# Optimization experiments

Hardware: AMD Instinct MI355X
Metric: run time of the kernel (lower is better)

## Reference

```python
import jax, jax.numpy as jnp
import numpy as np


def setup_inputs() -> dict:
    key = jax.random.key(0)
    ks = jax.random.split(key, 5)
    B, D, W = 8, 768, 128
    scale = 1.0 / np.sqrt(D)
    return {
        "x": jax.random.normal(ks[0], (B, D, W, W), dtype=jnp.float32),
        "in_proj_w": jax.random.normal(ks[1], (3 * D, D), dtype=jnp.float32) * scale,
        "in_proj_b": jax.random.normal(ks[2], (3 * D,), dtype=jnp.float32) * 0.01,
        "out_w": jax.random.normal(ks[3], (D, D), dtype=jnp.float32) * scale,
        "out_b": jax.random.normal(ks[4], (D,), dtype=jnp.float32) * 0.01,
        "num_heads": 12,
        "num_tokens": 8,
    }


def reference(x, in_proj_w, in_proj_b, out_w, out_b, num_heads, num_tokens):
    B, D, Wd, Hd = x.shape
    nt = num_tokens
    gs = Hd // nt            # grid (block) size
    T = nt * nt              # number of blocks / queries
    S = gs * gs              # k/v tokens per block
    h = num_heads
    hd = D // h

    # ---- query: adaptive avg pool to (nt, nt), flatten, permute -> (B, T, D)
    q = x.reshape(B, D, nt, gs, nt, gs).mean(axis=(3, 5))      # (B, D, nt, nt)
    q = q.reshape(B, D, T).transpose(0, 2, 1)                   # (B, T, D)

    # ---- key/value: faithful reproduction of unfold + view(x.size()) + reshape
    # torch: kv_perm (B,W,H,D) -> unfold -> (B, nt, nt, D, gs, gs) contiguous,
    # then reinterpreted flat as (B, W*H, D) (scrambles channel/pixel layout).
    t = x.transpose(0, 2, 3, 1)                                 # (B, W, H, D)
    t = t.reshape(B, nt, gs, nt, gs, D).transpose(0, 1, 3, 5, 2, 4)  # (B,nt,nt,D,gs,gs)
    kv = t.reshape(B, T, S, D)                                  # chunked into T blocks of S tokens

    # ---- in-projections (torch MultiheadAttention packed weights)
    Wq, Wk, Wv = in_proj_w[:D], in_proj_w[D:2 * D], in_proj_w[2 * D:]
    bq, bk, bv = in_proj_b[:D], in_proj_b[D:2 * D], in_proj_b[2 * D:]
    qp = (q @ Wq.T + bq).reshape(B, T, h, hd)                   # (B, T, h, hd)
    kp = (kv @ Wk.T + bk).reshape(B, T, S, h, hd)               # (B, T, S, h, hd)
    vp = (kv @ Wv.T + bv).reshape(B, T, S, h, hd)

    # ---- block-local single-query attention, batched over all T blocks
    scores = jnp.einsum("bthd,btshd->bths", qp, kp) / np.sqrt(hd)  # (B, T, h, S)
    attn = jax.nn.softmax(scores, axis=-1)
    ctx = jnp.einsum("bths,btshd->bthd", attn, vp).reshape(B, T, D)

    # ---- out projection
    return ctx @ out_w.T + out_b                                # (B, T, D)
```

## Files before the change

kernel.cpp:

```cpp
#include <hip/hip_runtime.h>
#include <hip/hip_bf16.h>

#define D_ 768
#define W_ 128
#define T_ 64
#define S_ 256
#define H_ 12
#define BT_ 512

__device__ __forceinline__ unsigned short f2bf(float f) {
  unsigned u = __float_as_uint(f);
  u = (u + 0x7FFFu + ((u >> 16) & 1u)) >> 16;
  return (unsigned short)u;
}

__global__ __launch_bounds__(512) void k_pack(const float* __restrict__ x,
                                              unsigned short* __restrict__ packed,
                                              float* __restrict__ q) {
  const int blk  = blockIdx.x;
  const int cc   = blk & 15;
  const int tjp  = (blk >> 4) & 3;
  const int ti   = (blk >> 6) & 7;
  const int b    = blk >> 9;
  const int tid  = threadIdx.x;
  const int w    = tid >> 6, lane = tid & 63;
  const int btg0 = b*64 + ti*8 + tjp*2;
  const int ch0  = cc * 48;

  __shared__ unsigned short tile[48][2][260];
  __shared__ float poolacc[48][2][2];

  const float* xrow = x + (size_t)b*D_*16384 + (16*ti)*128 + 32*tjp;

  #pragma unroll
  for (int it = 0; it < 12; ++it) {
    const int idx = it*512 + tid;
    const int c8 = idx & 7;
    const int r  = (idx >> 3) & 15;
    const int ch = idx >> 7;
    const float4 v = *(const float4*)(xrow + (size_t)(ch0 + ch)*16384 + r*128 + c8*4);
    const int btl = c8 >> 2;
    const int px  = r*16 + (c8 & 3)*4;
    unsigned lo = (unsigned)f2bf(v.x) | ((unsigned)f2bf(v.y) << 16);
    unsigned hi = (unsigned)f2bf(v.z) | ((unsigned)f2bf(v.w) << 16);
    *(uint2*)&tile[ch][btl][px] = make_uint2(lo, hi);
    float ps = (v.x + v.y) + (v.z + v.w);
    ps += __shfl_xor(ps, 1);
    ps += __shfl_xor(ps, 2);
    ps += __shfl_xor(ps, 8);
    ps += __shfl_xor(ps, 16);
    ps += __shfl_xor(ps, 32);
    if (lane == 0 || lane == 4) {
      const int chw = it*4 + (w >> 1);
      const int hwv = w & 1;
      poolacc[chw][lane >> 2][hwv] = ps;
    }
  }
  __syncthreads();

  {
    const int btl = tid >> 8, p = tid & 255;
    unsigned short* pbt = packed + ((size_t)(btg0 + btl)*16 + cc)*D_*16;
    #pragma unroll
    for (int c = 0; c < 3; ++c) {
      unsigned u[8];
      #pragma unroll
      for (int k2 = 0; k2 < 8; ++k2) {
        const unsigned a  = tile[3*(2*k2)     + c][btl][p];
        const unsigned b2 = tile[3*(2*k2 + 1) + c][btl][p];
        u[k2] = a | (b2 << 16);
      }
      unsigned short* dst = pbt + (size_t)(c*256 + p)*16;
      *(uint4*)(dst)     = make_uint4(u[0], u[1], u[2], u[3]);
      *(uint4*)(dst + 8) = make_uint4(u[4], u[5], u[6], u[7]);
    }
    if (tid < 96) {
      const int ch = tid >> 1, bl = tid & 1;
      q[(size_t)(btg0 + bl)*D_ + ch0 + ch] =
          (poolacc[ch][bl][0] + poolacc[ch][bl][1]) * (1.0f/256.0f);
    }
  }
}

__global__ __launch_bounds__(256) void k_qp(const float* __restrict__ q,
                                            const float* __restrict__ ipw,
                                            const float* __restrict__ ipb,
                                            float* __restrict__ qp) {
  const int jt = blockIdx.x >> 5;
  const int bt0 = (blockIdx.x & 31) * 16;
  const int tid = threadIdx.x;
  const float* Wr = ipw + (size_t)jt*64*D_;
  __shared__ float wt[64][65];
  __shared__ float at[16][65];
  const int i = tid & 63, qw = tid >> 6;
  float acc[4] = {0,0,0,0};
  for (int dc = 0; dc < D_; dc += 64) {
    #pragma unroll
    for (int k = 0; k < 4; ++k) {
      const int idx = k*256 + tid;
      const int r = idx >> 4, c4 = idx & 15;
      *(float4*)&wt[r][c4*4] = *(const float4*)(Wr + (size_t)r*D_ + dc + c4*4);
    }
    {
      const int r = tid >> 4, c4 = tid & 15;
      *(float4*)&at[r][c4*4] = *(const float4*)(q + (size_t)(bt0 + r)*D_ + dc + c4*4);
    }
    __syncthreads();
    #pragma unroll
    for (int dd = 0; dd < 64; ++dd) {
      const float wv = wt[i][dd];
      #pragma unroll
      for (int k = 0; k < 4; ++k)
        acc[k] += at[qw + k*4][dd] * wv;
    }
    __syncthreads();
  }
  const float bqv = ipb[jt*64 + i];
  #pragma unroll
  for (int k = 0; k < 4; ++k)
    qp[(size_t)(bt0 + qw + k*4)*D_ + jt*64 + i] = acc[k] + bqv;
}

__global__ __launch_bounds__(256) void k_fold(const float* __restrict__ qp,
                                              const float* __restrict__ ipw,
                                              float* __restrict__ qkout) {
  const int btc = blockIdx.x & 15;
  const int nt  = blockIdx.x >> 4;
  const int h   = nt / 12;
  const int ddc = (nt % 12) * 64;
  const int bt0 = btc * 32;
  const int tid = threadIdx.x;
  __shared__ float qpl[32][68];
  __shared__ float wkl[64][68];
  #pragma unroll
  for (int k = 0; k < 2; ++k) {
    const int idx = k*256 + tid;
    const int r = idx >> 4, c4 = idx & 15;
    *(float4*)&qpl[r][c4*4] = *(const float4*)(qp + (size_t)(bt0 + r)*D_ + h*64 + c4*4);
  }
  #pragma unroll
  for (int k = 0; k < 4; ++k) {
    const int idx = k*256 + tid;
    const int r = idx >> 4, c4 = idx & 15;
    *(float4*)&wkl[r][c4*4] = *(const float4*)(ipw + (size_t)(D_ + h*64 + r)*D_ + ddc + c4*4);
  }
  __syncthreads();
  const int i = tid & 63, qw = tid >> 6;
  float acc[8] = {0,0,0,0,0,0,0,0};
  #pragma unroll 8
  for (int kk = 0; kk < 64; ++kk) {
    const float w = wkl[kk][i];
    #pragma unroll
    for (int k = 0; k < 8; ++k)
      acc[k] += qpl[qw + k*4][kk] * w;
  }
  #pragma unroll
  for (int k = 0; k < 8; ++k)
    qkout[((size_t)(bt0 + qw + k*4)*H_ + h)*D_ + ddc + i] = acc[k] * 0.125f;
}

__global__ __launch_bounds__(256) void k_attn3(const unsigned short* __restrict__ packed,
                                               const float* __restrict__ qkin,
                                               float* __restrict__ wout) {
  const int bt = blockIdx.x;
  const int tid = threadIdx.x;
  const int wv = tid >> 6, lane = tid & 63;
  __shared__ float qk_lds[H_*D_];
  __shared__ float sc[H_][S_];

  {
    const float4* src = (const float4*)(qkin + (size_t)bt*H_*D_);
    float4* dst = (float4*)qk_lds;
    #pragma unroll
    for (int k = 0; k < 9; ++k) dst[k*256 + tid] = src[k*256 + tid];
  }
  __syncthreads();

  float acc[H_][4];
  #pragma unroll
  for (int h = 0; h < H_; ++h)
    #pragma unroll
    for (int j = 0; j < 4; ++j) acc[h][j] = 0.f;

  {
    const unsigned short* pb = packed + ((size_t)bt*16 + (lane >> 2))*D_*16 + (lane & 3)*4;
    const int d0 = wv * 192;
    #pragma unroll 4
    for (int d4 = 0; d4 < 48; ++d4) {
      const int d = d0 + d4*4;
      float f[4][4];
      #pragma unroll
      for (int dd = 0; dd < 4; ++dd) {
        const short4 pv = *(const short4*)(pb + (size_t)(d + dd)*16);
        f[dd][0] = __uint_as_float(((unsigned)(unsigned short)pv.x) << 16);
        f[dd][1] = __uint_as_float(((unsigned)(unsigned short)pv.y) << 16);
        f[dd][2] = __uint_as_float(((unsigned)(unsigned short)pv.z) << 16);
        f[dd][3] = __uint_as_float(((unsigned)(unsigned short)pv.w) << 16);
      }
      #pragma unroll
      for (int h = 0; h < H_; ++h) {
        const float4 qv = *(const float4*)&qk_lds[h*D_ + d];
        #pragma unroll
        for (int j = 0; j < 4; ++j)
          acc[h][j] += qv.x*f[0][j] + qv.y*f[1][j] + qv.z*f[2][j] + qv.w*f[3][j];
      }
    }
  }
  __syncthreads();

  if (wv == 0) {
    #pragma unroll
    for (int h = 0; h < H_; ++h)
      *(float4*)&sc[h][lane*4] = make_float4(acc[h][0], acc[h][1], acc[h][2], acc[h][3]);
  } else {
    float* dstp = qk_lds + (size_t)(wv - 1)*(H_*S_);
    #pragma unroll
    for (int h = 0; h < H_; ++h)
      *(float4*)&dstp[h*S_ + lane*4] = make_float4(acc[h][0], acc[h][1], acc[h][2], acc[h][3]);
  }
  __syncthreads();
  #pragma unroll
  for (int h = 0; h < H_; ++h)
    sc[h][tid] += qk_lds[0*(H_*S_) + h*S_ + tid]
                + qk_lds[1*(H_*S_) + h*S_ + tid]
                + qk_lds[2*(H_*S_) + h*S_ + tid];
  __syncthreads();

  {
    #pragma unroll
    for (int hh = 0; hh < 3; ++hh) {
      const int h = wv*3 + hh;
      float4 v = *(const float4*)(&sc[h][lane*4]);
      float m = fmaxf(fmaxf(v.x, v.y), fmaxf(v.z, v.w));
      #pragma unroll
      for (int off = 32; off > 0; off >>= 1) m = fmaxf(m, __shfl_xor(m, off));
      const float e0 = __expf(v.x - m), e1 = __expf(v.y - m),
                  e2 = __expf(v.z - m), e3 = __expf(v.w - m);
      float ss = (e0+e1)+(e2+e3);
      #pragma unroll
      for (int off = 32; off > 0; off >>= 1) ss += __shfl_xor(ss, off);
      const float inv = 1.0f / ss;
      *(float4*)(&sc[h][lane*4]) = make_float4(e0*inv, e1*inv, e2*inv, e3*inv);
    }
  }
  __syncthreads();

  float wacc[H_][3];
  #pragma unroll
  for (int h = 0; h < H_; ++h) { wacc[h][0]=0.f; wacc[h][1]=0.f; wacc[h][2]=0.f; }
  const unsigned short* prow = packed + (size_t)bt*16*D_*16;
  #pragma unroll 2
  for (int s8 = 0; s8 < 32; ++s8) {
    float f[3][8];
    #pragma unroll
    for (int c = 0; c < 3; ++c) {
      const uint4 pv = *(const uint4*)(prow + ((size_t)(s8 >> 1)*D_ + c*256 + tid)*16
                                            + (s8 & 1)*8);
      f[c][0] = __uint_as_float(pv.x << 16);
      f[c][1] = __uint_as_float(pv.x & 0xFFFF0000u);
      f[c][2] = __uint_as_float(pv.y << 16);
      f[c][3] = __uint_as_float(pv.y & 0xFFFF0000u);
      f[c][4] = __uint_as_float(pv.z << 16);
      f[c][5] = __uint_as_float(pv.z & 0xFFFF0000u);
      f[c][6] = __uint_as_float(pv.w << 16);
      f[c][7] = __uint_as_float(pv.w & 0xFFFF0000u);
    }
    #pragma unroll
    for (int h = 0; h < H_; ++h) {
      const float4 a0 = *(const float4*)&sc[h][s8*8];
      const float4 a1 = *(const float4*)&sc[h][s8*8 + 4];
      #pragma unroll
      for (int c = 0; c < 3; ++c)
        wacc[h][c] += a0.x*f[c][0] + a0.y*f[c][1] + a0.z*f[c][2] + a0.w*f[c][3]
                    + a1.x*f[c][4] + a1.y*f[c][5] + a1.z*f[c][6] + a1.w*f[c][7];
    }
  }
  float* wp = wout + (size_t)bt*H_*D_;
  #pragma unroll
  for (int h = 0; h < H_; ++h)
    #pragma unroll
    for (int c = 0; c < 3; ++c)
      wp[h*D_ + c*256 + tid] = wacc[h][c];
}

__global__ __launch_bounds__(256) void k_q(const float* __restrict__ x, float* __restrict__ q) {
  const int bd = blockIdx.x;
  const int tid = threadIdx.x;
  const float4* xp = (const float4*)(x + (size_t)bd * (W_*W_));
  float acc[8] = {0,0,0,0,0,0,0,0};
  #pragma unroll
  for (int k = 0; k < 16; ++k) {
    float4 v = xp[k*256 + tid];
    acc[k>>1] += (v.x + v.y) + (v.z + v.w);
  }
  __shared__ float part[256][9];
  #pragma unroll
  for (int i = 0; i < 8; ++i) part[tid][i] = acc[i];
  __syncthreads();
  if (tid < 64) {
    const int ti = tid >> 3, tj = tid & 7;
    float s = 0.f;
    #pragma unroll
    for (int m = 0; m < 8; ++m)
      #pragma unroll
      for (int n = 0; n < 4; ++n)
        s += part[m*32 + tj*4 + n][ti];
    const int b = bd / D_, d = bd - b*D_;
    q[(size_t)(b*T_ + tid)*D_ + d] = s * (1.0f/256.0f);
  }
}

__global__ __launch_bounds__(256) void k_attn(const float* __restrict__ x,
                                              const float* __restrict__ qkin,
                                              float* __restrict__ wout) {
  const int bt = blockIdx.x;
  const int b = bt >> 6, t = bt & 63;
  const int ti = t >> 3, tj = t & 7;
  const int tid = threadIdx.x;
  __shared__ float qkl[H_*D_];
  __shared__ float sc[H_][S_];
  const float* xb = x + (size_t)b*D_*W_*W_ + ti*16*W_ + tj*16;
  {
    const float4* src = (const float4*)(qkin + (size_t)bt*H_*D_);
    float4* dst = (float4*)qkl;
    #pragma unroll
    for (int k = 0; k < 9; ++k) dst[k*256 + tid] = src[k*256 + tid];
  }
  __syncthreads();
  float acc[H_];
  #pragma unroll
  for (int h = 0; h < H_; ++h) acc[h] = 0.f;
  #pragma unroll
  for (int c = 0; c < 3; ++c) {
    const float* chp = xb + (size_t)(3*tid + c)*(W_*W_);
    for (int blk = 0; blk < 8; ++blk) {
      float4 v[8];
      #pragma unroll
      for (int u = 0; u < 8; ++u) {
        const int pg = blk*8 + u;
        v[u] = *(const float4*)(chp + (pg>>2)*W_ + (pg&3)*4);
      }
      const int dbase = c*256 + blk*32;
      #pragma unroll
      for (int h = 0; h < H_; ++h) {
        const float4* qh = (const float4*)(qkl + h*D_ + dbase);
        float s0 = 0.f;
        #pragma unroll
        for (int u = 0; u < 8; ++u) {
          const float4 qq = qh[u];
          s0 += qq.x*v[u].x + qq.y*v[u].y + qq.z*v[u].z + qq.w*v[u].w;
        }
        acc[h] += s0;
      }
    }
  }
  #pragma unroll
  for (int h = 0; h < H_; ++h) sc[h][tid] = acc[h];
  __syncthreads();
  {
    const int wv = tid >> 6, lane = tid & 63;
    #pragma unroll
    for (int hh = 0; hh < 3; ++hh) {
      const int h = wv*3 + hh;
      float4 v = *(const float4*)(&sc[h][lane*4]);
      float m = fmaxf(fmaxf(v.x, v.y), fmaxf(v.z, v.w));
      #pragma unroll
      for (int off = 32; off > 0; off >>= 1) m = fmaxf(m, __shfl_xor(m, off));
      const float e0 = __expf(v.x - m), e1 = __expf(v.y - m),
                  e2 = __expf(v.z - m), e3 = __expf(v.w - m);
      float ss = (e0+e1)+(e2+e3);
      #pragma unroll
      for (int off = 32; off > 0; off >>= 1) ss += __shfl_xor(ss, off);
      const float inv = 1.0f / ss;
      *(float4*)(&sc[h][lane*4]) = make_float4(e0*inv, e1*inv, e2*inv, e3*inv);
    }
  }
  __syncthreads();
  float wacc[H_][3];
  #pragma unroll
  for (int h = 0; h < H_; ++h) { wacc[h][0]=0.f; wacc[h][1]=0.f; wacc[h][2]=0.f; }
  const float* xp0 = xb + (tid>>4)*W_ + (tid&15);
  for (int s = 0; s < S_; ++s) {
    const float p0 = xp0[(size_t)(3*s+0)*(W_*W_)];
    const float p1 = xp0[(size_t)(3*s+1)*(W_*W_)];
    const float p2 = xp0[(size_t)(3*s+2)*(W_*W_)];
    #pragma unroll
    for (int h = 0; h < H_; ++h) {
      const float at = sc[h][s];
      wacc[h][0] += at*p0; wacc[h][1] += at*p1; wacc[h][2] += at*p2;
    }
  }
  float* wp = wout + (size_t)bt*H_*D_;
  #pragma unroll
  for (int h = 0; h < H_; ++h)
    #pragma unroll
    for (int c = 0; c < 3; ++c)
      wp[h*D_ + c*256 + tid] = wacc[h][c];
}

__global__ __launch_bounds__(256) void k_ctx(const float* __restrict__ wbuf,
                                             const float* __restrict__ ipw,
                                             const float* __restrict__ ipb,
                                             float* __restrict__ ctx) {
  const int h = blockIdx.x >> 5;
  const int bt0 = (blockIdx.x & 31) * 16;
  const int tid = threadIdx.x;
  const float* Wv = ipw + (size_t)2*D_*D_ + (size_t)h*64*D_;
  __shared__ float wt[64][65];
  __shared__ float at[16][65];
  const int i = tid & 63, qw = tid >> 6;
  float acc[4] = {0,0,0,0};
  for (int dc = 0; dc < D_; dc += 64) {
    #pragma unroll
    for (int k = 0; k < 4; ++k) {
      const int idx = k*256 + tid;
      const int r = idx >> 4, c4 = idx & 15;
      *(float4*)&wt[r][c4*4] = *(const float4*)(Wv + (size_t)r*D_ + dc + c4*4);
    }
    {
      const int r = tid >> 4, c4 = tid & 15;
      *(float4*)&at[r][c4*4] = *(const float4*)(wbuf + ((size_t)(bt0 + r)*H_ + h)*D_ + dc + c4*4);
    }
    __syncthreads();
    #pragma unroll
    for (int dd = 0; dd < 64; ++dd) {
      const float wv = wt[i][dd];
      #pragma unroll
      for (int k = 0; k < 4; ++k)
        acc[k] += at[qw + k*4][dd] * wv;
    }
    __syncthreads();
  }
  const float bvv = ipb[2*D_ + h*64 + i];
  #pragma unroll
  for (int k = 0; k < 4; ++k)
    ctx[(size_t)(bt0 + qw + k*4)*D_ + h*64 + i] = acc[k] + bvv;
}

__global__ __launch_bounds__(256) void k_out(const float* __restrict__ ctx,
                                             const float* __restrict__ ow,
                                             const float* __restrict__ ob,
                                             float* __restrict__ out) {
  const int jt = blockIdx.x >> 5;
  const int bt0 = (blockIdx.x & 31) * 16;
  const int tid = threadIdx.x;
  const float* Wr = ow + (size_t)jt*64*D_;
  __shared__ float wt[64][65];
  __shared__ float at[16][65];
  const int i = tid & 63, qw = tid >> 6;
  float acc[4] = {0,0,0,0};
  for (int dc = 0; dc < D_; dc += 64) {
    #pragma unroll
    for (int k = 0; k < 4; ++k) {
      const int idx = k*256 + tid;
      const int r = idx >> 4, c4 = idx & 15;
      *(float4*)&wt[r][c4*4] = *(const float4*)(Wr + (size_t)r*D_ + dc + c4*4);
    }
    {
      const int r = tid >> 4, c4 = tid & 15;
      *(float4*)&at[r][c4*4] = *(const float4*)(ctx + (size_t)(bt0 + r)*D_ + dc + c4*4);
    }
    __syncthreads();
    #pragma unroll
    for (int dd = 0; dd < 64; ++dd) {
      const float wv = wt[i][dd];
      #pragma unroll
      for (int k = 0; k < 4; ++k)
        acc[k] += at[qw + k*4][dd] * wv;
    }
    __syncthreads();
  }
  const float obv = ob[jt*64 + i];
  #pragma unroll
  for (int k = 0; k < 4; ++k)
    out[(size_t)(bt0 + qw + k*4)*D_ + jt*64 + i] = acc[k] + obv;
}

extern "C" void kernel_launch(void* const* d_in, const int* in_sizes, int n_in,
                              void* d_out, int out_size, void* d_ws, size_t ws_size,
                              hipStream_t stream) {
  const float* x   = (const float*)d_in[0];
  const float* ipw = (const float*)d_in[1];
  const float* ipb = (const float*)d_in[2];
  const float* ow  = (const float*)d_in[3];
  const float* ob  = (const float*)d_in[4];
  float* out = (float*)d_out;

  float* q    = (float*)d_ws;
  float* qp   = q    + (size_t)BT_*D_;
  float* qk   = qp   + (size_t)BT_*D_;
  float* wb   = qk   + (size_t)BT_*H_*D_;
  float* ctxb = wb   + (size_t)BT_*H_*D_;
  unsigned short* packed = (unsigned short*)(ctxb + (size_t)BT_*D_);

  const size_t need_main = ((size_t)BT_*D_*3 + (size_t)BT_*H_*D_*2) * 4
                         + (size_t)BT_*D_*S_*2;

  if (ws_size >= need_main) {
    k_pack <<<dim3(4096), dim3(512), 0, stream>>>(x, packed, q);
    k_qp   <<<dim3(384),  dim3(256), 0, stream>>>(q, ipw, ipb, qp);
    k_fold <<<dim3(2304), dim3(256), 0, stream>>>(qp, ipw, qk);
    k_attn3<<<dim3(BT_),  dim3(256), 0, stream>>>(packed, qk, wb);
    k_ctx  <<<dim3(384),  dim3(256), 0, stream>>>(wb, ipw, ipb, ctxb);
    k_out  <<<dim3(384),  dim3(256), 0, stream>>>(ctxb, ow, ob, out);
  } else {
    k_q    <<<dim3(8*D_), dim3(256), 0, stream>>>(x, q);
    k_qp   <<<dim3(384),  dim3(256), 0, stream>>>(q, ipw, ipb, qp);
    k_fold <<<dim3(2304), dim3(256), 0, stream>>>(qp, ipw, qk);
    k_attn <<<dim3(BT_),  dim3(256), 0, stream>>>(x, qk, wb);
    k_ctx  <<<dim3(384),  dim3(256), 0, stream>>>(wb, ipw, ipb, ctxb);
    k_out  <<<dim3(384),  dim3(256), 0, stream>>>(ctxb, ow, ob, out);
  }
}
```

Baseline: 413.0 us.

## Split attention heads across two blocks, store folded queries as bf16, simplify pack

The attention kernel now handles six heads per block and launches twice as many blocks. This raises occupancy through lower register and LDS use per block and spreads the work over more CUs, at the cost of reading the packed K/V stream twice. The folded query-key vectors are stored as bf16 to halve that traffic and are expanded to fp32 in LDS, which adds a rounding error. The pack kernel is reworked so each thread owns one channel column, uses 384 threads and pools with fewer shuffles.

```diff
diff --git a/kernel.cpp b/kernel.cpp
--- a/kernel.cpp
+++ b/kernel.cpp
@@ -6,6 +6,7 @@
 #define T_ 64
 #define S_ 256
 #define H_ 12
+#define HH_ 6
 #define BT_ 512
 
 __device__ __forceinline__ unsigned short f2bf(float f) {
@@ -13,8 +14,11 @@
   u = (u + 0x7FFFu + ((u >> 16) & 1u)) >> 16;
   return (unsigned short)u;
 }
-
-__global__ __launch_bounds__(512) void k_pack(const float* __restrict__ x,
+__device__ __forceinline__ float bfu(unsigned s) {
+  return __uint_as_float(s << 16);
+}
+
+__global__ __launch_bounds__(384) void k_pack(const float* __restrict__ x,
                                               unsigned short* __restrict__ packed,
                                               float* __restrict__ q) {
   const int blk  = blockIdx.x;
@@ -23,62 +27,53 @@
   const int ti   = (blk >> 6) & 7;
   const int b    = blk >> 9;
   const int tid  = threadIdx.x;
-  const int w    = tid >> 6, lane = tid & 63;
+  const int c8   = tid & 7;
+  const int ch   = tid >> 3;
+  const int btl  = c8 >> 2;
   const int btg0 = b*64 + ti*8 + tjp*2;
   const int ch0  = cc * 48;
 
   __shared__ unsigned short tile[48][2][260];
-  __shared__ float poolacc[48][2][2];
-
-  const float* xrow = x + (size_t)b*D_*16384 + (16*ti)*128 + 32*tjp;
-
-  #pragma unroll
-  for (int it = 0; it < 12; ++it) {
-    const int idx = it*512 + tid;
-    const int c8 = idx & 7;
-    const int r  = (idx >> 3) & 15;
-    const int ch = idx >> 7;
-    const float4 v = *(const float4*)(xrow + (size_t)(ch0 + ch)*16384 + r*128 + c8*4);
-    const int btl = c8 >> 2;
-    const int px  = r*16 + (c8 & 3)*4;
+  __shared__ float poolsc[48][2];
+
+  const float* xcol = x + (size_t)b*D_*16384 + (size_t)(ch0 + ch)*16384
+                        + (16*ti)*128 + 32*tjp + c8*4;
+
+  float psum = 0.f;
+  #pragma unroll
+  for (int r = 0; r < 16; ++r) {
+    const float4 v = *(const float4*)(xcol + r*128);
+    const int px = r*16 + (c8 & 3)*4;
     unsigned lo = (unsigned)f2bf(v.x) | ((unsigned)f2bf(v.y) << 16);
     unsigned hi = (unsigned)f2bf(v.z) | ((unsigned)f2bf(v.w) << 16);
     *(uint2*)&tile[ch][btl][px] = make_uint2(lo, hi);
-    float ps = (v.x + v.y) + (v.z + v.w);
-    ps += __shfl_xor(ps, 1);
-    ps += __shfl_xor(ps, 2);
-    ps += __shfl_xor(ps, 8);
-    ps += __shfl_xor(ps, 16);
-    ps += __shfl_xor(ps, 32);
-    if (lane == 0 || lane == 4) {
-      const int chw = it*4 + (w >> 1);
-      const int hwv = w & 1;
-      poolacc[chw][lane >> 2][hwv] = ps;
-    }
-  }
-  __syncthreads();
-
-  {
-    const int btl = tid >> 8, p = tid & 255;
-    unsigned short* pbt = packed + ((size_t)(btg0 + btl)*16 + cc)*D_*16;
+    psum += (v.x + v.y) + (v.z + v.w);
+  }
+  psum += __shfl_xor(psum, 1);
+  psum += __shfl_xor(psum, 2);
+  if ((c8 & 3) == 0) poolsc[ch][btl] = psum;
+  __syncthreads();
+
+  for (int ii = tid; ii < 512; ii += 384) {
+    const int bl = ii >> 8, p = ii & 255;
+    unsigned short* pbt = packed + ((size_t)(btg0 + bl)*16 + cc)*D_*16;
     #pragma unroll
     for (int c = 0; c < 3; ++c) {
       unsigned u[8];
       #pragma unroll
       for (int k2 = 0; k2 < 8; ++k2) {
-        const unsigned a  = tile[3*(2*k2)     + c][btl][p];
-        const unsigned b2 = tile[3*(2*k2 + 1) + c][btl][p];
+        const unsigned a  = tile[3*(2*k2)     + c][bl][p];
+        const unsigned b2 = tile[3*(2*k2 + 1) + c][bl][p];
         u[k2] = a | (b2 << 16);
       }
       unsigned short* dst = pbt + (size_t)(c*256 + p)*16;
       *(uint4*)(dst)     = make_uint4(u[0], u[1], u[2], u[3]);
       *(uint4*)(dst + 8) = make_uint4(u[4], u[5], u[6], u[7]);
     }
-    if (tid < 96) {
-      const int ch = tid >> 1, bl = tid & 1;
-      q[(size_t)(btg0 + bl)*D_ + ch0 + ch] =
-          (poolacc[ch][bl][0] + poolacc[ch][bl][1]) * (1.0f/256.0f);
-    }
+  }
+  if (tid < 96) {
+    const int ch2 = tid >> 1, bl = tid & 1;
+    q[(size_t)(btg0 + bl)*D_ + ch0 + ch2] = poolsc[ch2][bl] * (1.0f/256.0f);
   }
 }
 
@@ -123,7 +118,7 @@
 
 __global__ __launch_bounds__(256) void k_fold(const float* __restrict__ qp,
                                               const float* __restrict__ ipw,
-                                              float* __restrict__ qkout) {
+                                              unsigned short* __restrict__ qkout) {
   const int btc = blockIdx.x & 15;
   const int nt  = blockIdx.x >> 4;
   const int h   = nt / 12;
@@ -156,29 +151,39 @@
   }
   #pragma unroll
   for (int k = 0; k < 8; ++k)
-    qkout[((size_t)(bt0 + qw + k*4)*H_ + h)*D_ + ddc + i] = acc[k] * 0.125f;
+    qkout[((size_t)(bt0 + qw + k*4)*H_ + h)*D_ + ddc + i] = f2bf(acc[k] * 0.125f);
 }
 
 __global__ __launch_bounds__(256) void k_attn3(const unsigned short* __restrict__ packed,
-                                               const float* __restrict__ qkin,
+                                               const unsigned short* __restrict__ qkin,
                                                float* __restrict__ wout) {
-  const int bt = blockIdx.x;
+  const int hg = blockIdx.x >> 9;
+  const int bt = blockIdx.x & 511;
   const int tid = threadIdx.x;
   const int wv = tid >> 6, lane = tid & 63;
-  __shared__ float qk_lds[H_*D_];
-  __shared__ float sc[H_][S_];
+  __shared__ float pool_lds[HH_ * D_];
+  __shared__ float sc[HH_][S_];
 
   {
-    const float4* src = (const float4*)(qkin + (size_t)bt*H_*D_);
-    float4* dst = (float4*)qk_lds;
-    #pragma unroll
-    for (int k = 0; k < 9; ++k) dst[k*256 + tid] = src[k*256 + tid];
-  }
-  __syncthreads();
-
-  float acc[H_][4];
-  #pragma unroll
-  for (int h = 0; h < H_; ++h)
+    const uint4* src = (const uint4*)(qkin + ((size_t)bt*H_ + hg*HH_)*D_);
+    #pragma unroll
+    for (int k = 0; k < 3; ++k) {
+      const int idx = k*256 + tid;
+      if (idx < 576) {
+        const uint4 v = src[idx];
+        float* d = pool_lds + idx*8;
+        d[0] = bfu(v.x & 0xFFFFu); d[1] = bfu(v.x >> 16);
+        d[2] = bfu(v.y & 0xFFFFu); d[3] = bfu(v.y >> 16);
+        d[4] = bfu(v.z & 0xFFFFu); d[5] = bfu(v.z >> 16);
+        d[6] = bfu(v.w & 0xFFFFu); d[7] = bfu(v.w >> 16);
+      }
+    }
+  }
+  __syncthreads();
+
+  float acc[HH_][4];
+  #pragma unroll
+  for (int h = 0; h < HH_; ++h)
     #pragma unroll
     for (int j = 0; j < 4; ++j) acc[h][j] = 0.f;
 
@@ -192,14 +197,14 @@
       #pragma unroll
       for (int dd = 0; dd < 4; ++dd) {
         const short4 pv = *(const short4*)(pb + (size_t)(d + dd)*16);
-        f[dd][0] = __uint_as_float(((unsigned)(unsigned short)pv.x) << 16);
-        f[dd][1] = __uint_as_float(((unsigned)(unsigned short)pv.y) << 16);
-        f[dd][2] = __uint_as_float(((unsigned)(unsigned short)pv.z) << 16);
-        f[dd][3] = __uint_as_float(((unsigned)(unsigned short)pv.w) << 16);
-      }
-      #pragma unroll
-      for (int h = 0; h < H_; ++h) {
-        const float4 qv = *(const float4*)&qk_lds[h*D_ + d];
+        f[dd][0] = bfu((unsigned)(unsigned short)pv.x);
+        f[dd][1] = bfu((unsigned)(unsigned short)pv.y);
+        f[dd][2] = bfu((unsigned)(unsigned short)pv.z);
+        f[dd][3] = bfu((unsigned)(unsigned short)pv.w);
+      }
+      #pragma unroll
+      for (int h = 0; h < HH_; ++h) {
+        const float4 qv = *(const float4*)&pool_lds[h*D_ + d];
         #pragma unroll
         for (int j = 0; j < 4; ++j)
           acc[h][j] += qv.x*f[0][j] + qv.y*f[1][j] + qv.z*f[2][j] + qv.w*f[3][j];
@@ -210,26 +215,26 @@
 
   if (wv == 0) {
     #pragma unroll
-    for (int h = 0; h < H_; ++h)
+    for (int h = 0; h < HH_; ++h)
       *(float4*)&sc[h][lane*4] = make_float4(acc[h][0], acc[h][1], acc[h][2], acc[h][3]);
   } else {
-    float* dstp = qk_lds + (size_t)(wv - 1)*(H_*S_);
-    #pragma unroll
-    for (int h = 0; h < H_; ++h)
+    float* dstp = pool_lds + (size_t)(wv - 1)*(HH_*S_);
+    #pragma unroll
+    for (int h = 0; h < HH_; ++h)
       *(float4*)&dstp[h*S_ + lane*4] = make_float4(acc[h][0], acc[h][1], acc[h][2], acc[h][3]);
   }
   __syncthreads();
   #pragma unroll
-  for (int h = 0; h < H_; ++h)
-    sc[h][tid] += qk_lds[0*(H_*S_) + h*S_ + tid]
-                + qk_lds[1*(H_*S_) + h*S_ + tid]
-                + qk_lds[2*(H_*S_) + h*S_ + tid];
-  __syncthreads();
-
-  {
-    #pragma unroll
-    for (int hh = 0; hh < 3; ++hh) {
-      const int h = wv*3 + hh;
+  for (int h = 0; h < HH_; ++h)
+    sc[h][tid] += pool_lds[0*(HH_*S_) + h*S_ + tid]
+                + pool_lds[1*(HH_*S_) + h*S_ + tid]
+                + pool_lds[2*(HH_*S_) + h*S_ + tid];
+  __syncthreads();
+
+  if (wv < 3) {
+    #pragma unroll
+    for (int hh = 0; hh < 2; ++hh) {
+      const int h = wv*2 + hh;
       float4 v = *(const float4*)(&sc[h][lane*4]);
       float m = fmaxf(fmaxf(v.x, v.y), fmaxf(v.z, v.w));
       #pragma unroll
@@ -245,9 +250,9 @@
   }
   __syncthreads();
 
-  float wacc[H_][3];
-  #pragma unroll
-  for (int h = 0; h < H_; ++h) { wacc[h][0]=0.f; wacc[h][1]=0.f; wacc[h][2]=0.f; }
+  float wacc[HH_][3];
+  #pragma unroll
+  for (int h = 0; h < HH_; ++h) { wacc[h][0]=0.f; wacc[h][1]=0.f; wacc[h][2]=0.f; }
   const unsigned short* prow = packed + (size_t)bt*16*D_*16;
   #pragma unroll 2
   for (int s8 = 0; s8 < 32; ++s8) {
@@ -256,17 +261,13 @@
     for (int c = 0; c < 3; ++c) {
       const uint4 pv = *(const uint4*)(prow + ((size_t)(s8 >> 1)*D_ + c*256 + tid)*16
                                             + (s8 & 1)*8);
-      f[c][0] = __uint_as_float(pv.x << 16);
-      f[c][1] = __uint_as_float(pv.x & 0xFFFF0000u);
-      f[c][2] = __uint_as_float(pv.y << 16);
-      f[c][3] = __uint_as_float(pv.y & 0xFFFF0000u);
-      f[c][4] = __uint_as_float(pv.z << 16);
-      f[c][5] = __uint_as_float(pv.z & 0xFFFF0000u);
-      f[c][6] = __uint_as_float(pv.w << 16);
-      f[c][7] = __uint_as_float(pv.w & 0xFFFF0000u);
-    }
-    #pragma unroll
-    for (int h = 0; h < H_; ++h) {
+      f[c][0] = bfu(pv.x & 0xFFFFu); f[c][1] = bfu(pv.x >> 16);
+      f[c][2] = bfu(pv.y & 0xFFFFu); f[c][3] = bfu(pv.y >> 16);
+      f[c][4] = bfu(pv.z & 0xFFFFu); f[c][5] = bfu(pv.z >> 16);
+      f[c][6] = bfu(pv.w & 0xFFFFu); f[c][7] = bfu(pv.w >> 16);
+    }
+    #pragma unroll
+    for (int h = 0; h < HH_; ++h) {
       const float4 a0 = *(const float4*)&sc[h][s8*8];
       const float4 a1 = *(const float4*)&sc[h][s8*8 + 4];
       #pragma unroll
@@ -275,9 +276,9 @@
                     + a1.x*f[c][4] + a1.y*f[c][5] + a1.z*f[c][6] + a1.w*f[c][7];
     }
   }
-  float* wp = wout + (size_t)bt*H_*D_;
-  #pragma unroll
-  for (int h = 0; h < H_; ++h)
+  float* wp = wout + ((size_t)bt*H_ + hg*HH_)*D_;
+  #pragma unroll
+  for (int h = 0; h < HH_; ++h)
     #pragma unroll
     for (int c = 0; c < 3; ++c)
       wp[h*D_ + c*256 + tid] = wacc[h][c];
@@ -311,7 +312,7 @@
 }
 
 __global__ __launch_bounds__(256) void k_attn(const float* __restrict__ x,
-                                              const float* __restrict__ qkin,
+                                              const unsigned short* __restrict__ qkin,
                                               float* __restrict__ wout) {
   const int bt = blockIdx.x;
   const int b = bt >> 6, t = bt & 63;
@@ -321,10 +322,19 @@
   __shared__ float sc[H_][S_];
   const float* xb = x + (size_t)b*D_*W_*W_ + ti*16*W_ + tj*16;
   {
-    const float4* src = (const float4*)(qkin + (size_t)bt*H_*D_);
-    float4* dst = (float4*)qkl;
-    #pragma unroll
-    for (int k = 0; k < 9; ++k) dst[k*256 + tid] = src[k*256 + tid];
+    const uint4* src = (const uint4*)(qkin + (size_t)bt*H_*D_);
+    #pragma unroll
+    for (int k = 0; k < 5; ++k) {
+      const int idx = k*256 + tid;
+      if (idx < 1152) {
+        const uint4 v = src[idx];
+        float* d = qkl + idx*8;
+        d[0] = bfu(v.x & 0xFFFFu); d[1] = bfu(v.x >> 16);
+        d[2] = bfu(v.y & 0xFFFFu); d[3] = bfu(v.y >> 16);
+        d[4] = bfu(v.z & 0xFFFFu); d[5] = bfu(v.z >> 16);
+        d[6] = bfu(v.w & 0xFFFFu); d[7] = bfu(v.w >> 16);
+      }
+    }
   }
   __syncthreads();
   float acc[H_];
@@ -488,8 +498,8 @@
 
   float* q    = (float*)d_ws;
   float* qp   = q    + (size_t)BT_*D_;
-  float* qk   = qp   + (size_t)BT_*D_;
-  float* wb   = qk   + (size_t)BT_*H_*D_;
+  unsigned short* qk = (unsigned short*)(qp + (size_t)BT_*D_);
+  float* wb   = qp   + (size_t)BT_*D_ + (size_t)BT_*H_*D_;
   float* ctxb = wb   + (size_t)BT_*H_*D_;
   unsigned short* packed = (unsigned short*)(ctxb + (size_t)BT_*D_);
 
@@ -497,10 +507,10 @@
                          + (size_t)BT_*D_*S_*2;
 
   if (ws_size >= need_main) {
-    k_pack <<<dim3(4096), dim3(512), 0, stream>>>(x, packed, q);
+    k_pack <<<dim3(4096), dim3(384), 0, stream>>>(x, packed, q);
     k_qp   <<<dim3(384),  dim3(256), 0, stream>>>(q, ipw, ipb, qp);
     k_fold <<<dim3(2304), dim3(256), 0, stream>>>(qp, ipw, qk);
-    k_attn3<<<dim3(BT_),  dim3(256), 0, stream>>>(packed, qk, wb);
+    k_attn3<<<dim3(1024), dim3(256), 0, stream>>>(packed, qk, wb);
     k_ctx  <<<dim3(384),  dim3(256), 0, stream>>>(wb, ipw, ipb, ctxb);
     k_out  <<<dim3(384),  dim3(256), 0, stream>>>(ctxb, ow, ob, out);
   } else {
```

Result: faster. 393.9 us (-4.6%).
